# Kernel tuning notes

Measured on AMD Instinct MI355X. Metric: run time of the kernel, lower is better.

## Reference

```python
import jax, jax.numpy as jnp
import numpy as np

V, D, N = 1_000_000, 128, 262_144  # vocab rows, embed dim, gradient rows


def setup_inputs() -> dict:
    key = jax.random.key(0)
    k1, k2, k3, k4 = jax.random.split(key, 4)
    weights = jax.random.normal(k1, (V, D), dtype=jnp.float32) * 0.01
    moments = jnp.zeros((V, D), dtype=jnp.float32)
    gradients = jax.random.normal(k2, (N, D), dtype=jnp.float32) * 0.01
    indices = jax.random.randint(k3, (N,), 0, V, dtype=jnp.int64)
    learning_rate = jax.random.uniform(k4, (1,), dtype=jnp.float32) * 0.1
    valid_count = 200_000  # static python int: number of valid gradient rows
    return {
        "gradients": gradients,
        "weights": weights,
        "moments": moments,
        "indices": indices,
        "learning_rate": learning_rate,
        "valid_count": valid_count,
    }


def reference(gradients, weights, moments, indices, learning_rate, valid_count):
    """Sparse SGD table update with valid-count masking.

    For i < valid_count: weights[indices[i]] -= lr * gradients[i].
    Duplicate indices accumulate (scatter-add), matching sequential
    row-wise SGD updates. Moments are passed through unchanged
    (plain SGD formulation of the Habana sparse-SGD op).
    """
    lr = learning_rate[0]
    # mask out padded gradient rows (i >= valid_count)
    valid = jnp.arange(gradients.shape[0]) < valid_count  # [N]
    g = jnp.where(valid[:, None], gradients, jnp.zeros((), gradients.dtype))
    weights_out = weights.at[indices].add(-lr * g)  # scatter-add update
    moments_out = moments
    return weights_out, moments_out
```

## Files before the change

kernel.cpp:

```cpp
#include <hip/hip_runtime.h>


#define D_DIM 128

__global__ void sgd_scatter_kernel(const float* __restrict__ grads,
                                   const int* __restrict__ indices,
                                   const float* __restrict__ lr_ptr,
                                   const int* __restrict__ vc_ptr,
                                   float* __restrict__ w_out) {
    const float lr = lr_ptr[0];
    const long long total = (long long)vc_ptr[0] * D_DIM;
    const long long stride = (long long)gridDim.x * blockDim.x;
    for (long long t = (long long)blockIdx.x * blockDim.x + threadIdx.x;
         t < total; t += stride) {
        const int i = (int)(t >> 7);
        const int j = (int)(t & 127);
        const long long row = (long long)indices[i];
        atomicAdd(w_out + row * D_DIM + j, -lr * grads[t]);
    }
}

extern "C" void kernel_launch(void* const* d_in, const int* in_sizes, int n_in,
                              void* d_out, int out_size, void* d_ws, size_t ws_size,
                              hipStream_t stream) {
    const float* grads   = (const float*)d_in[0];
    const float* weights = (const float*)d_in[1];
    const float* moments = (const float*)d_in[2];
    const int*   indices = (const int*)  d_in[3];
    const float* lr_ptr  = (const float*)d_in[4];
    const int*   vc_ptr  = (const int*)  d_in[5];

    const size_t VD = (size_t)in_sizes[1];
    float* w_out = (float*)d_out;
    float* m_out = w_out + VD;

    hipMemcpyAsync(w_out, weights, VD * sizeof(float), hipMemcpyDeviceToDevice, stream);
    hipMemcpyAsync(m_out, moments, VD * sizeof(float), hipMemcpyDeviceToDevice, stream);

    const int blocks = 8192, threads = 256;
    sgd_scatter_kernel<<<blocks, threads, 0, stream>>>(grads, indices, lr_ptr, vc_ptr, w_out);
}
```

Before: 1.765 ms.

## Replace atomic scatter with per-row linked-list gather fused into table copy

Builds per-row linked lists of gradient indices using atomicExch on a head array in workspace. A fused kernel then copies moments and weights row by row, applying all gradients for each row in registers before writing. This removes the separate weight copy pass and the float atomics into the table. It adds an init pass over V ints and a dependent-load chain walk per row. Summation order for duplicate indices becomes nondeterministic.

```diff
diff --git a/kernel.cpp b/kernel.cpp
--- a/kernel.cpp
+++ b/kernel.cpp
@@ -2,6 +2,59 @@
 
 
 #define D_DIM 128
+
+
+__global__ __launch_bounds__(256) void init_head_kernel(int* __restrict__ head,
+                                                        const int V) {
+    const int stride = gridDim.x * blockDim.x;
+    for (int v = blockIdx.x * blockDim.x + threadIdx.x; v < V; v += stride)
+        head[v] = -1;
+}
+
+__global__ __launch_bounds__(256) void build_chains_kernel(
+    const int* __restrict__ indices,
+    const int* __restrict__ vc_ptr,
+    int* __restrict__ head,
+    int* __restrict__ next) {
+    const int i = blockIdx.x * blockDim.x + threadIdx.x;
+    if (i < vc_ptr[0]) {
+        const int row = indices[i];
+        next[i] = atomicExch(&head[row], i);
+    }
+}
+
+__global__ __launch_bounds__(256) void fused_copy_update_kernel(
+    const float* __restrict__ weights,
+    const float* __restrict__ moments,
+    const float* __restrict__ grads,
+    const float* __restrict__ lr_ptr,
+    const int* __restrict__ head,
+    const int* __restrict__ next,
+    float* __restrict__ w_out,
+    float* __restrict__ m_out,
+    const int V) {
+    const float lr = lr_ptr[0];
+    const int lane2 = (threadIdx.x & 63) * 2;
+    const int wpb = blockDim.x >> 6;
+    const int wave = blockIdx.x * wpb + (threadIdx.x >> 6);
+    const int nwaves = gridDim.x * wpb;
+
+    for (int row = wave; row < V; row += nwaves) {
+        const size_t base = (size_t)row * D_DIM + lane2;
+
+        const float2 m = *(const float2*)(moments + base);
+        *(float2*)(m_out + base) = m;
+
+        float2 w = *(const float2*)(weights + base);
+        for (int i = head[row]; i >= 0; i = next[i]) {
+            const float2 g = *(const float2*)(grads + (size_t)i * D_DIM + lane2);
+            w.x = fmaf(-lr, g.x, w.x);
+            w.y = fmaf(-lr, g.y, w.y);
+        }
+        *(float2*)(w_out + base) = w;
+    }
+}
+
 
 __global__ void sgd_scatter_kernel(const float* __restrict__ grads,
                                    const int* __restrict__ indices,
@@ -31,12 +84,28 @@
     const int*   vc_ptr  = (const int*)  d_in[5];
 
     const size_t VD = (size_t)in_sizes[1];
+    const int V = (int)(VD / D_DIM);
+    const int N = in_sizes[0] / D_DIM;
     float* w_out = (float*)d_out;
     float* m_out = w_out + VD;
 
-    hipMemcpyAsync(w_out, weights, VD * sizeof(float), hipMemcpyDeviceToDevice, stream);
-    hipMemcpyAsync(m_out, moments, VD * sizeof(float), hipMemcpyDeviceToDevice, stream);
+    const size_t ws_need = ((size_t)V + (size_t)N) * sizeof(int);
 
-    const int blocks = 8192, threads = 256;
-    sgd_scatter_kernel<<<blocks, threads, 0, stream>>>(grads, indices, lr_ptr, vc_ptr, w_out);
+    if (d_ws != nullptr && ws_size >= ws_need) {
+        int* head = (int*)d_ws;
+        int* next = head + V;
+
+        init_head_kernel<<<1024, 256, 0, stream>>>(head, V);
+        build_chains_kernel<<<(N + 255) / 256, 256, 0, stream>>>(
+            indices, vc_ptr, head, next);
+        fused_copy_update_kernel<<<2048, 256, 0, stream>>>(
+            weights, moments, grads, lr_ptr, head, next, w_out, m_out, V);
+    } else {
+        hipMemcpyAsync(w_out, weights, VD * sizeof(float),
+                       hipMemcpyDeviceToDevice, stream);
+        hipMemcpyAsync(m_out, moments, VD * sizeof(float),
+                       hipMemcpyDeviceToDevice, stream);
+        sgd_scatter_kernel<<<8192, 256, 0, stream>>>(grads, indices, lr_ptr,
+                                                     vc_ptr, w_out);
+    }
 }
```

Measured after the change: 1.738 ms. About the same (-1.5%).
